# Kernel optimization log

Measured on AMD Instinct MI355X. Metric: run time of the kernel, lower is better.

The kernel has to match this reference:

```python
import jax, jax.numpy as jnp
import numpy as np

N_NODES = 50000


def _gcn_layer(x, src, dst, deg_inv_sqrt, W, b):
    # GCNConv (PyG defaults): h = x @ W; out = D^-1/2 (A+I) D^-1/2 h + b
    h = x @ W
    norm = deg_inv_sqrt[src] * deg_inv_sqrt[dst]          # [E]
    msg = h[src] * norm[:, None]                           # [E, d_out]
    agg = jax.ops.segment_sum(msg, dst, num_segments=N_NODES)
    agg = agg + h * (deg_inv_sqrt * deg_inv_sqrt)[:, None]  # self-loop term
    return agg + b


def _stack(x, src, dst, dis, W1, b1, W2, b2, W3, b3):
    h = jax.nn.relu(_gcn_layer(x, src, dst, dis, W1, b1))
    h = jax.nn.relu(_gcn_layer(h, src, dst, dis, W2, b2))
    return jax.nn.relu(_gcn_layer(h, src, dst, dis, W3, b3))


def setup_inputs() -> dict:
    key = jax.random.key(0)
    ks = jax.random.split(key, 16)
    din, lat, E = 128, 64, 800000
    x = jax.random.normal(ks[0], (N_NODES, din), dtype=jnp.float32)
    edge_index = jax.random.randint(ks[1], (2, E), 0, N_NODES, dtype=jnp.int64)

    def lin(k, fan_in, fan_out):
        s = 1.0 / np.sqrt(fan_in)
        kw, kb = jax.random.split(k)
        W = jax.random.uniform(kw, (fan_in, fan_out), minval=-s, maxval=s, dtype=jnp.float32)
        b = jax.random.uniform(kb, (fan_out,), minval=-s, maxval=s, dtype=jnp.float32)
        return W, b

    Wm1, bm1 = lin(ks[2], din, 64)
    Wm2, bm2 = lin(ks[3], 64, 128)
    Wm3, bm3 = lin(ks[4], 128, lat)
    Wl1, bl1 = lin(ks[5], din, 64)
    Wl2, bl2 = lin(ks[6], 64, 128)
    Wl3, bl3 = lin(ks[7], 128, lat)
    return {"x": x, "edge_index": edge_index,
            "Wm1": Wm1, "bm1": bm1, "Wm2": Wm2, "bm2": bm2, "Wm3": Wm3, "bm3": bm3,
            "Wl1": Wl1, "bl1": bl1, "Wl2": Wl2, "bl2": bl2, "Wl3": Wl3, "bl3": bl3}


def reference(x, edge_index, Wm1, bm1, Wm2, bm2, Wm3, bm3, Wl1, bl1, Wl2, bl2, Wl3, bl3):
    src, dst = edge_index[0], edge_index[1]
    # degree with self-loops (PyG: deg over dst of A+I)
    deg = jax.ops.segment_sum(jnp.ones_like(dst, dtype=x.dtype), dst, num_segments=N_NODES) + 1.0
    dis = jax.lax.rsqrt(deg)
    mu = _stack(x, src, dst, dis, Wm1, bm1, Wm2, bm2, Wm3, bm3)
    log = _stack(x, src, dst, dis, Wl1, bl1, Wl2, bl2, Wl3, bl3)
    return (mu, log)
```

## Files before the change

### kernel.cpp

```cpp
#include <hip/hip_runtime.h>

#define N_NODES_C 50000

__global__ void detect_kernel(const int* __restrict__ w, int ncheck, int* __restrict__ flag) {
    int tid = blockIdx.x * blockDim.x + threadIdx.x;
    if (tid < ncheck) {
        if (w[2 * tid + 1] != 0) *flag = 0;
    }
}

__global__ void count_kernel(const int* __restrict__ ei, int E, const int* __restrict__ flag,
                             int* __restrict__ counts) {
    int e = blockIdx.x * blockDim.x + threadIdx.x;
    if (e >= E) return;
    int shift = (*flag != 0) ? 1 : 0;
    int d = ei[(unsigned)(E + e) << shift];
    atomicAdd(&counts[d], 1);
}

__global__ void scan_kernel(const int* __restrict__ counts, int* __restrict__ row_start,
                            int* __restrict__ cursor, float* __restrict__ dis, int n) {
    __shared__ int wsum[16];
    __shared__ int carry;
    __shared__ int chunk_total;
    int tid = threadIdx.x;
    int lane = tid & 63;
    int wid = tid >> 6;
    if (tid == 0) carry = 0;
    __syncthreads();
    for (int base = 0; base < n; base += 1024) {
        int i = base + tid;
        int v = (i < n) ? counts[i] : 0;
        int x = v;
        #pragma unroll
        for (int off = 1; off < 64; off <<= 1) {
            int y = __shfl_up(x, off);
            if (lane >= off) x += y;
        }
        if (lane == 63) wsum[wid] = x;
        __syncthreads();
        if (tid == 0) {
            int run = 0;
            #pragma unroll
            for (int q = 0; q < 16; q++) { int t = wsum[q]; wsum[q] = run; run += t; }
            chunk_total = run;
        }
        __syncthreads();
        int excl = x - v + wsum[wid] + carry;
        if (i < n) {
            row_start[i] = excl;
            cursor[i] = excl;
            dis[i] = rsqrtf((float)v + 1.0f);
        }
        __syncthreads();
        if (tid == 0) carry += chunk_total;
        __syncthreads();
    }
    if (tid == 0) row_start[n] = carry;
}

__global__ void fill_kernel(const int* __restrict__ ei, int E, const int* __restrict__ flag,
                            int* __restrict__ cursor, int* __restrict__ csr_src) {
    int e = blockIdx.x * blockDim.x + threadIdx.x;
    if (e >= E) return;
    int shift = (*flag != 0) ? 1 : 0;
    int s = ei[(unsigned)e << shift];
    int d = ei[(unsigned)(E + e) << shift];
    int pos = atomicAdd(&cursor[d], 1);
    csr_src[pos] = s;
}

template <bool FINAL>
__global__ __launch_bounds__(256) void agg128_kernel(const float* __restrict__ h,
                                                     const int* __restrict__ row_start,
                                                     const int* __restrict__ csr_src,
                                                     const float* __restrict__ dis,
                                                     const float* __restrict__ bmu,
                                                     const float* __restrict__ blog,
                                                     float* __restrict__ out,
                                                     float* __restrict__ outlog, int M) {
    int wid = threadIdx.x >> 6;
    int lane = threadIdx.x & 63;
    int node = blockIdx.x * 4 + wid;
    if (node >= M) return;
    int half = lane >> 5;
    int c0 = (lane & 31) * 4;

    int s = row_start[node];
    int e = row_start[node + 1];
    float dn = dis[node];

    float a0 = 0.f, a1 = 0.f, a2 = 0.f, a3 = 0.f;
    int i = s + half;
    for (; i + 6 < e; i += 8) {
        int s0 = csr_src[i];
        int s1 = csr_src[i + 2];
        int s2 = csr_src[i + 4];
        int s3 = csr_src[i + 6];
        float w0 = dis[s0] * dn;
        float w1 = dis[s1] * dn;
        float w2 = dis[s2] * dn;
        float w3 = dis[s3] * dn;
        float4 v0 = *(const float4*)&h[(size_t)s0 * 128 + c0];
        float4 v1 = *(const float4*)&h[(size_t)s1 * 128 + c0];
        float4 v2 = *(const float4*)&h[(size_t)s2 * 128 + c0];
        float4 v3 = *(const float4*)&h[(size_t)s3 * 128 + c0];
        a0 = fmaf(w0, v0.x, a0); a1 = fmaf(w0, v0.y, a1);
        a2 = fmaf(w0, v0.z, a2); a3 = fmaf(w0, v0.w, a3);
        a0 = fmaf(w1, v1.x, a0); a1 = fmaf(w1, v1.y, a1);
        a2 = fmaf(w1, v1.z, a2); a3 = fmaf(w1, v1.w, a3);
        a0 = fmaf(w2, v2.x, a0); a1 = fmaf(w2, v2.y, a1);
        a2 = fmaf(w2, v2.z, a2); a3 = fmaf(w2, v2.w, a3);
        a0 = fmaf(w3, v3.x, a0); a1 = fmaf(w3, v3.y, a1);
        a2 = fmaf(w3, v3.z, a2); a3 = fmaf(w3, v3.w, a3);
    }
    for (; i < e; i += 2) {
        int s0 = csr_src[i];
        float w0 = dis[s0] * dn;
        float4 v0 = *(const float4*)&h[(size_t)s0 * 128 + c0];
        a0 = fmaf(w0, v0.x, a0); a1 = fmaf(w0, v0.y, a1);
        a2 = fmaf(w0, v0.z, a2); a3 = fmaf(w0, v0.w, a3);
    }
    a0 += __shfl_xor(a0, 32);
    a1 += __shfl_xor(a1, 32);
    a2 += __shfl_xor(a2, 32);
    a3 += __shfl_xor(a3, 32);

    float sw = dn * dn;
    float4 sv = *(const float4*)&h[(size_t)node * 128 + c0];
    a0 = fmaf(sw, sv.x, a0); a1 = fmaf(sw, sv.y, a1);
    a2 = fmaf(sw, sv.z, a2); a3 = fmaf(sw, sv.w, a3);

    if (half == 0) {
        if constexpr (FINAL) {
            float b0, b1, b2, b3;
            float* yp;
            if (c0 < 64) {
                b0 = bmu[c0]; b1 = bmu[c0 + 1]; b2 = bmu[c0 + 2]; b3 = bmu[c0 + 3];
                yp = out + (size_t)node * 64 + c0;
            } else {
                int c = c0 - 64;
                b0 = blog[c]; b1 = blog[c + 1]; b2 = blog[c + 2]; b3 = blog[c + 3];
                yp = outlog + (size_t)node * 64 + c;
            }
            float4 o;
            o.x = fmaxf(a0 + b0, 0.f);
            o.y = fmaxf(a1 + b1, 0.f);
            o.z = fmaxf(a2 + b2, 0.f);
            o.w = fmaxf(a3 + b3, 0.f);
            *(float4*)yp = o;
        } else {
            *(float4*)&out[(size_t)node * 128 + c0] = make_float4(a0, a1, a2, a3);
        }
    }
}

template <int K, int LDX, int XA, int XB, int N, int BM, int KCH, int NT,
          bool RELU, bool BIAS>
__global__ __launch_bounds__(NT) void gemm4_kernel(const float* __restrict__ X,
                                                   const float* __restrict__ Wa,
                                                   const float* __restrict__ Wb,
                                                   const float* __restrict__ ba,
                                                   const float* __restrict__ bb,
                                                   float* __restrict__ Y, int ldy, int M) {
    constexpr int NTX = N / 8;
    constexpr int NTY = NT / NTX;
    constexpr int RPT = BM / NTY;
    constexpr int NH = N / 2;
    constexpr bool SHARED = (XA == XB);
    constexpr int NS = SHARED ? 1 : 2;
    constexpr int RS = NS * KCH + 1;
    constexpr int TPB = NTX / 2;
    static_assert(RPT == 8, "micro-tile must be 8x8");

    __shared__ float xs[BM * RS];
    __shared__ float ws[KCH * N];

    int t = threadIdx.x;
    int row0 = blockIdx.x * BM;
    int tx = t % NTX;
    int ty = t / NTX;

    int cb, cst, xslot;
    if constexpr (SHARED) {
        cb = tx; cst = NTX; xslot = 0;
    } else {
        int branch = tx / TPB;
        int txl = tx - branch * TPB;
        cb = branch * NH + txl;
        cst = TPB;
        xslot = branch;
    }

    float acc[RPT][8];
    #pragma unroll
    for (int rr = 0; rr < RPT; rr++)
        #pragma unroll
        for (int j = 0; j < 8; j++) acc[rr][j] = 0.f;

    for (int kc = 0; kc < K; kc += KCH) {
        __syncthreads();
        for (int i = t; i < BM * NS * KCH; i += NT) {
            int r = i / (NS * KCH), cc = i % (NS * KCH);
            int slot = cc / KCH, kk = cc - slot * KCH;
            int gcol = (slot ? XB : XA) + kc + kk;
            int row = row0 + r;
            float v = (row < M) ? X[(size_t)row * LDX + gcol] : 0.f;
            xs[r * RS + cc] = v;
        }
        for (int i = t; i < KCH * N; i += NT) {
            int kk = i / N, c = i - kk * N;
            float v = (c < NH) ? Wa[(size_t)(kc + kk) * NH + c]
                               : Wb[(size_t)(kc + kk) * NH + (c - NH)];
            ws[kk * N + c] = v;
        }
        __syncthreads();

        #pragma unroll 2
        for (int kk = 0; kk < KCH; ++kk) {
            float wv[8];
            #pragma unroll
            for (int j = 0; j < 8; j++) wv[j] = ws[kk * N + cb + j * cst];
            float xv[RPT];
            #pragma unroll
            for (int rr = 0; rr < RPT; rr++)
                xv[rr] = xs[(ty + rr * NTY) * RS + xslot * KCH + kk];
            #pragma unroll
            for (int rr = 0; rr < RPT; rr++)
                #pragma unroll
                for (int j = 0; j < 8; j++)
                    acc[rr][j] = fmaf(xv[rr], wv[j], acc[rr][j]);
        }
    }

    float bj[8];
    #pragma unroll
    for (int j = 0; j < 8; j++) {
        if constexpr (BIAS) {
            int c = cb + j * cst;
            bj[j] = (c < NH) ? ba[c] : bb[c - NH];
        } else {
            bj[j] = 0.f;
        }
    }
    #pragma unroll
    for (int rr = 0; rr < RPT; rr++) {
        int row = row0 + ty + rr * NTY;
        if (row < M) {
            float* yp = Y + (size_t)row * ldy;
            #pragma unroll
            for (int j = 0; j < 8; j++) {
                float o = acc[rr][j] + bj[j];
                if constexpr (RELU) o = fmaxf(o, 0.f);
                yp[cb + j * cst] = o;
            }
        }
    }
}

extern "C" void kernel_launch(void* const* d_in, const int* in_sizes, int n_in,
                              void* d_out, int out_size, void* d_ws, size_t ws_size,
                              hipStream_t stream) {
    const float* x   = (const float*)d_in[0];
    const int*   ei  = (const int*)d_in[1];
    const float* Wm1 = (const float*)d_in[2];  const float* bm1 = (const float*)d_in[3];
    const float* Wm2 = (const float*)d_in[4];  const float* bm2 = (const float*)d_in[5];
    const float* Wm3 = (const float*)d_in[6];  const float* bm3 = (const float*)d_in[7];
    const float* Wl1 = (const float*)d_in[8];  const float* bl1 = (const float*)d_in[9];
    const float* Wl2 = (const float*)d_in[10]; const float* bl2 = (const float*)d_in[11];
    const float* Wl3 = (const float*)d_in[12]; const float* bl3 = (const float*)d_in[13];
    float* out = (float*)d_out;

    const int M = N_NODES_C;
    const int E = in_sizes[1] / 2;

    char* ws = (char*)d_ws;
    size_t off = 0;
    auto alloc = [&](size_t bytes) {
        size_t o = off;
        off += (bytes + 255) & ~(size_t)255;
        return o;
    };
    int*   flag      = (int*)(ws + alloc(4));
    int*   counts    = (int*)(ws + alloc((size_t)M * 4));
    int*   row_start = (int*)(ws + alloc((size_t)(M + 1) * 4));
    int*   cursor    = (int*)(ws + alloc((size_t)M * 4));
    float* dis       = (float*)(ws + alloc((size_t)M * 4));
    int*   csr_src   = (int*)(ws + alloc((size_t)E * 4));
    float* bufA      = (float*)(ws + alloc((size_t)M * 256 * 4));
    float* bufB      = (float*)(ws + alloc((size_t)M * 256 * 4));

    hipMemsetAsync(flag, 1, 4, stream);
    hipMemsetAsync(counts, 0, (size_t)M * 4, stream);

    int ncheck = (E < 2048) ? E : 2048;
    detect_kernel<<<(ncheck + 255) / 256, 256, 0, stream>>>(ei, ncheck, flag);
    count_kernel<<<(E + 255) / 256, 256, 0, stream>>>(ei, E, flag, counts);
    scan_kernel<<<1, 1024, 0, stream>>>(counts, row_start, cursor, dis, M);
    fill_kernel<<<(E + 255) / 256, 256, 0, stream>>>(ei, E, flag, cursor, csr_src);

    int ablocks = (M + 3) / 4;

    agg128_kernel<false><<<ablocks, 256, 0, stream>>>(x, row_start, csr_src, dis,
                                                      nullptr, nullptr, bufA, nullptr, M);

    gemm4_kernel<128, 128, 0, 0, 128, 128, 32, 256, true, true>
        <<<(M + 127) / 128, 256, 0, stream>>>(bufA, Wm1, Wl1, bm1, bl1, bufB, 128, M);

    agg128_kernel<false><<<ablocks, 256, 0, stream>>>(bufB, row_start, csr_src, dis,
                                                      nullptr, nullptr, bufA, nullptr, M);

    gemm4_kernel<64, 128, 0, 64, 256, 64, 32, 256, true, true>
        <<<(M + 63) / 64, 256, 0, stream>>>(bufA, Wm2, Wl2, bm2, bl2, bufB, 256, M);

    gemm4_kernel<128, 256, 0, 128, 128, 128, 32, 256, false, false>
        <<<(M + 127) / 128, 256, 0, stream>>>(bufB, Wm3, Wl3, nullptr, nullptr, bufA, 128, M);

    agg128_kernel<true><<<ablocks, 256, 0, stream>>>(bufA, row_start, csr_src, dis,
                                                     bm3, bl3, out, out + (size_t)M * 64, M);
}
```

Before: 590.1 us.

## Redesign GEMM micro-tiling with padded shared memory and float4 X reads

```diff
diff --git a/kernel.cpp b/kernel.cpp
--- a/kernel.cpp
+++ b/kernel.cpp
@@ -157,91 +157,95 @@
 
 template <int K, int LDX, int XA, int XB, int N, int BM, int KCH, int NT,
           bool RELU, bool BIAS>
-__global__ __launch_bounds__(NT) void gemm4_kernel(const float* __restrict__ X,
+__global__ __launch_bounds__(NT) void gemm5_kernel(const float* __restrict__ X,
                                                    const float* __restrict__ Wa,
                                                    const float* __restrict__ Wb,
                                                    const float* __restrict__ ba,
                                                    const float* __restrict__ bb,
                                                    float* __restrict__ Y, int ldy, int M) {
-    constexpr int NTX = N / 8;
+    constexpr bool SHARED = (XA == XB);
+    constexpr int NTX = 16;
     constexpr int NTY = NT / NTX;
     constexpr int RPT = BM / NTY;
+    constexpr int CPT = N / NTX;
     constexpr int NH = N / 2;
-    constexpr bool SHARED = (XA == XB);
     constexpr int NS = SHARED ? 1 : 2;
-    constexpr int RS = NS * KCH + 1;
-    constexpr int TPB = NTX / 2;
-    static_assert(RPT == 8, "micro-tile must be 8x8");
+    constexpr int RS = NS * KCH + 4;
+    constexpr int NHP = NH + 16;
+    constexpr int ROWW = SHARED ? N : 2 * NHP;
+    constexpr int CST = SHARED ? 16 : 8;
+    static_assert(KCH == 16, "bank design assumes KCH=16");
+    static_assert(NT == 256, "bank design assumes NT=256");
+    static_assert(SHARED ? (N % 32 == 0) : true, "shared ws stride");
 
     __shared__ float xs[BM * RS];
-    __shared__ float ws[KCH * N];
+    __shared__ float ws[KCH * ROWW];
 
     int t = threadIdx.x;
     int row0 = blockIdx.x * BM;
-    int tx = t % NTX;
-    int ty = t / NTX;
-
-    int cb, cst, xslot;
-    if constexpr (SHARED) {
-        cb = tx; cst = NTX; xslot = 0;
-    } else {
-        int branch = tx / TPB;
-        int txl = tx - branch * TPB;
-        cb = branch * NH + txl;
-        cst = TPB;
-        xslot = branch;
-    }
-
-    float acc[RPT][8];
+    int tx = t & 15;
+    int ty = t >> 4;
+    int branch = SHARED ? 0 : (tx >> 3);
+    int txl = SHARED ? tx : (tx & 7);
+    int wbase = SHARED ? tx : (branch * NHP + txl);
+    int xsoff = branch * KCH;
+
+    float acc[RPT][CPT];
     #pragma unroll
     for (int rr = 0; rr < RPT; rr++)
         #pragma unroll
-        for (int j = 0; j < 8; j++) acc[rr][j] = 0.f;
+        for (int j = 0; j < CPT; j++) acc[rr][j] = 0.f;
 
     for (int kc = 0; kc < K; kc += KCH) {
         __syncthreads();
         for (int i = t; i < BM * NS * KCH; i += NT) {
             int r = i / (NS * KCH), cc = i % (NS * KCH);
-            int slot = cc / KCH, kk = cc - slot * KCH;
-            int gcol = (slot ? XB : XA) + kc + kk;
+            int gcol = ((cc >= KCH) ? XB : XA) + kc + (cc & (KCH - 1));
             int row = row0 + r;
-            float v = (row < M) ? X[(size_t)row * LDX + gcol] : 0.f;
-            xs[r * RS + cc] = v;
+            xs[r * RS + cc] = (row < M) ? X[(size_t)row * LDX + gcol] : 0.f;
         }
         for (int i = t; i < KCH * N; i += NT) {
             int kk = i / N, c = i - kk * N;
             float v = (c < NH) ? Wa[(size_t)(kc + kk) * NH + c]
                                : Wb[(size_t)(kc + kk) * NH + (c - NH)];
-            ws[kk * N + c] = v;
-        }
-        __syncthreads();
-
-        #pragma unroll 2
-        for (int kk = 0; kk < KCH; ++kk) {
-            float wv[8];
-            #pragma unroll
-            for (int j = 0; j < 8; j++) wv[j] = ws[kk * N + cb + j * cst];
-            float xv[RPT];
+            int a;
+            if constexpr (SHARED) a = kk * N + c;
+            else a = kk * ROWW + (c < NH ? c : NHP + (c - NH));
+            ws[a] = v;
+        }
+        __syncthreads();
+
+        #pragma unroll
+        for (int kk4 = 0; kk4 < KCH / 4; ++kk4) {
+            float4 xv[RPT];
             #pragma unroll
             for (int rr = 0; rr < RPT; rr++)
-                xv[rr] = xs[(ty + rr * NTY) * RS + xslot * KCH + kk];
+                xv[rr] = *(const float4*)&xs[(ty + rr * NTY) * RS + xsoff + 4 * kk4];
             #pragma unroll
-            for (int rr = 0; rr < RPT; rr++)
+            for (int dk = 0; dk < 4; ++dk) {
+                int kk = 4 * kk4 + dk;
+                float xk[RPT];
                 #pragma unroll
-                for (int j = 0; j < 8; j++)
-                    acc[rr][j] = fmaf(xv[rr], wv[j], acc[rr][j]);
-        }
-    }
-
-    float bj[8];
+                for (int rr = 0; rr < RPT; rr++)
+                    xk[rr] = (dk == 0) ? xv[rr].x : (dk == 1) ? xv[rr].y
+                           : (dk == 2) ? xv[rr].z : xv[rr].w;
+                #pragma unroll
+                for (int j = 0; j < CPT; ++j) {
+                    float w = ws[kk * ROWW + wbase + j * CST];
+                    #pragma unroll
+                    for (int rr = 0; rr < RPT; rr++)
+                        acc[rr][j] = fmaf(xk[rr], w, acc[rr][j]);
+                }
+            }
+        }
+    }
+
+    float bj[CPT];
     #pragma unroll
-    for (int j = 0; j < 8; j++) {
-        if constexpr (BIAS) {
-            int c = cb + j * cst;
-            bj[j] = (c < NH) ? ba[c] : bb[c - NH];
-        } else {
-            bj[j] = 0.f;
-        }
+    for (int j = 0; j < CPT; j++) {
+        int c = SHARED ? (tx + 16 * j) : (branch * NH + txl + 8 * j);
+        if constexpr (BIAS) bj[j] = (c < NH) ? ba[c] : bb[c - NH];
+        else bj[j] = 0.f;
     }
     #pragma unroll
     for (int rr = 0; rr < RPT; rr++) {
@@ -249,10 +253,11 @@
         if (row < M) {
             float* yp = Y + (size_t)row * ldy;
             #pragma unroll
-            for (int j = 0; j < 8; j++) {
+            for (int j = 0; j < CPT; j++) {
+                int c = SHARED ? (tx + 16 * j) : (branch * NH + txl + 8 * j);
                 float o = acc[rr][j] + bj[j];
                 if constexpr (RELU) o = fmaxf(o, 0.f);
-                yp[cb + j * cst] = o;
+                yp[c] = o;
             }
         }
     }
@@ -300,21 +305,22 @@
     fill_kernel<<<(E + 255) / 256, 256, 0, stream>>>(ei, E, flag, cursor, csr_src);
 
     int ablocks = (M + 3) / 4;
+    int gblocks = (M + 63) / 64;
 
     agg128_kernel<false><<<ablocks, 256, 0, stream>>>(x, row_start, csr_src, dis,
                                                       nullptr, nullptr, bufA, nullptr, M);
 
-    gemm4_kernel<128, 128, 0, 0, 128, 128, 32, 256, true, true>
-        <<<(M + 127) / 128, 256, 0, stream>>>(bufA, Wm1, Wl1, bm1, bl1, bufB, 128, M);
+    gemm5_kernel<128, 128, 0, 0, 128, 64, 16, 256, true, true>
+        <<<gblocks, 256, 0, stream>>>(bufA, Wm1, Wl1, bm1, bl1, bufB, 128, M);
 
     agg128_kernel<false><<<ablocks, 256, 0, stream>>>(bufB, row_start, csr_src, dis,
                                                       nullptr, nullptr, bufA, nullptr, M);
 
-    gemm4_kernel<64, 128, 0, 64, 256, 64, 32, 256, true, true>
-        <<<(M + 63) / 64, 256, 0, stream>>>(bufA, Wm2, Wl2, bm2, bl2, bufB, 256, M);
-
-    gemm4_kernel<128, 256, 0, 128, 128, 128, 32, 256, false, false>
-        <<<(M + 127) / 128, 256, 0, stream>>>(bufB, Wm3, Wl3, nullptr, nullptr, bufA, 128, M);
+    gemm5_kernel<64, 128, 0, 64, 256, 64, 16, 256, true, true>
+        <<<gblocks, 256, 0, stream>>>(bufA, Wm2, Wl2, bm2, bl2, bufB, 256, M);
+
+    gemm5_kernel<128, 256, 0, 128, 128, 64, 16, 256, false, false>
+        <<<gblocks, 256, 0, stream>>>(bufB, Wm3, Wl3, nullptr, nullptr, bufA, 128, M);
 
     agg128_kernel<true><<<ablocks, 256, 0, stream>>>(bufA, row_start, csr_src, dis,
                                                      bm3, bl3, out, out + (size_t)M * 64, M);
```

After: 594.8 us. Within noise of the previous version (+0.8%).
